# Kernel optimization log

Measured on AMD Instinct MI355X. Metric: run time of the kernel, lower is better.

## Reference

```python
import jax, jax.numpy as jnp
import numpy as np

N_ITEM = 50000
N_NODES = 2 * N_ITEM
NNZ = 3200000
EMB = 512
N_LAYERS = 3
BATCH = 4096
EPS = 1e-12


def setup_inputs() -> dict:
    key = jax.random.key(0)
    ks = jax.random.split(key, 12)
    s = 1.0 / np.sqrt(EMB)
    return {
        "all_vision": jax.random.normal(ks[0], (N_ITEM, EMB), jnp.float32) * s,
        "all_text": jax.random.normal(ks[1], (N_ITEM, EMB), jnp.float32) * s,
        "edge_row": jax.random.randint(ks[2], (NNZ,), 0, N_NODES, jnp.int32),
        "edge_col": jax.random.randint(ks[3], (NNZ,), 0, N_NODES, jnp.int32),
        "edge_val": jax.random.uniform(ks[4], (NNZ,), jnp.float32) * (1.0 / 32.0),
        "items": jax.random.randint(ks[5], (BATCH,), 0, N_ITEM, jnp.int32),
        "W_gc": jax.random.normal(ks[6], (N_LAYERS, EMB, EMB), jnp.float32) * s,
        "b_gc": jax.random.normal(ks[7], (N_LAYERS, EMB), jnp.float32) * 0.01,
        "W_gc2": jax.random.normal(ks[8], (N_LAYERS, EMB, EMB), jnp.float32) * s,
        "b_gc2": jax.random.normal(ks[9], (N_LAYERS, EMB), jnp.float32) * 0.01,
        "W_bi": jax.random.normal(ks[10], (N_LAYERS, EMB, EMB), jnp.float32) * s,
        "b_bi": jax.random.normal(ks[11], (N_LAYERS, EMB), jnp.float32) * 0.01,
    }


def reference(all_vision, all_text, edge_row, edge_col, edge_val, items,
              W_gc, b_gc, W_gc2, b_gc2, W_bi, b_bi):
    n = all_vision.shape[0]
    n_nodes = 2 * n

    def spmm(x):  # sparse [2N,2N] @ dense [2N,D] via gather + segment-sum
        return jax.ops.segment_sum(edge_val[:, None] * x[edge_col],
                                   edge_row, num_segments=n_nodes)

    ego = jnp.concatenate([all_vision, all_text], axis=0)   # [2N, D]
    oge = jnp.concatenate([all_text, all_vision], axis=0)   # fixed across layers
    acc = ego  # running sum over layer outputs (replaces stack+sum)
    for k in range(W_gc.shape[0]):
        side = spmm(ego)
        edis = spmm(oge)
        sum_e = side @ W_gc[k] + b_gc[k] + edis @ W_gc2[k] + b_gc2[k]
        bi = (ego * side + oge * edis) @ W_bi[k] + b_bi[k]
        ego = jax.nn.leaky_relu(sum_e + bi, negative_slope=0.2)
        # eval mode: message dropout is identity
        nrm = jnp.sqrt(jnp.sum(ego * ego, axis=1, keepdims=True))
        acc = acc + ego / jnp.maximum(nrm, EPS)  # F.normalize(p=2, dim=1)
    v_emb = acc[:n][items]
    t_emb = acc[n:][items]
    return (v_emb, t_emb)
```

## Files before the change

### kernel.cpp

```cpp
#include <hip/hip_runtime.h>
#include <stdint.h>

#define NITEM 50000
#define NN    100000
#define NNPAD 100352
#define CH    25088
#define NCH   4
#define EDGES 3200000
#define D     512
#define KCAT  1536
#define NL    3
#define BATCH 4096
#define NSEL  8192

typedef float  f32x4 __attribute__((ext_vector_type(4)));
typedef short  s16x8 __attribute__((ext_vector_type(8)));

__device__ __forceinline__ float bflo(unsigned u){ return __uint_as_float(u<<16); }
__device__ __forceinline__ float bfhi(unsigned u){ return __uint_as_float(u & 0xffff0000u); }
__device__ __forceinline__ float bf2f(unsigned short h){ return __uint_as_float(((unsigned)h)<<16); }
__device__ __forceinline__ unsigned short f2bf(float f){
  unsigned u = __float_as_uint(f);
  u += 0x7fffu + ((u>>16)&1u);
  return (unsigned short)(u>>16);
}
__device__ __forceinline__ void unpack8(uint4 d, float* f){
  f[0]=bflo(d.x); f[1]=bfhi(d.x);
  f[2]=bflo(d.y); f[3]=bfhi(d.y);
  f[4]=bflo(d.z); f[5]=bfhi(d.z);
  f[6]=bflo(d.w); f[7]=bfhi(d.w);
}
__device__ __forceinline__ uint4 pack8(const float* f){
  uint4 o;
  o.x = (unsigned)f2bf(f[0]) | ((unsigned)f2bf(f[1])<<16);
  o.y = (unsigned)f2bf(f[2]) | ((unsigned)f2bf(f[3])<<16);
  o.z = (unsigned)f2bf(f[4]) | ((unsigned)f2bf(f[5])<<16);
  o.w = (unsigned)f2bf(f[6]) | ((unsigned)f2bf(f[7])<<16);
  return o;
}
__device__ __forceinline__ void load8f(const void* base, size_t eoff, int isf32, float* f){
  if (isf32){
    const float* p = (const float*)base + eoff;
    f32x4 a = *(const f32x4*)p;
    f32x4 b = *(const f32x4*)(p + 4);
    f[0]=a[0]; f[1]=a[1]; f[2]=a[2]; f[3]=a[3];
    f[4]=b[0]; f[5]=b[1]; f[6]=b[2]; f[7]=b[3];
  } else {
    uint4 d = *(const uint4*)((const unsigned short*)base + eoff);
    unpack8(d, f);
  }
}
__device__ __forceinline__ float load1f(const void* base, size_t i, int isf32){
  return isf32 ? ((const float*)base)[i] : bf2f(((const unsigned short*)base)[i]);
}
__device__ __forceinline__ void gld_lds16(const void* g, void* l){
  __builtin_amdgcn_global_load_lds((__attribute__((address_space(1))) unsigned int*)(g),
                                   (__attribute__((address_space(3))) unsigned int*)(l),
                                   16, 0, 0);
}

__global__ void k_zero(int* __restrict__ p, int n){
  int i = blockIdx.x*256 + threadIdx.x;
  if (i < n) p[i] = 0;
}

__global__ void k_wsdbg(float* __restrict__ out, float mb, int n){
  int i = blockIdx.x*256 + threadIdx.x;
  if (i < n) out[i] = mb;
}

__global__ void k_detect(const unsigned short* __restrict__ vis, int* __restrict__ flag){
  __shared__ int cnt;
  if (threadIdx.x == 0) cnt = 0;
  __syncthreads();
  int c = 0;
  for (int i = threadIdx.x; i < 8192; i += 256){
    unsigned e = (vis[i] >> 7) & 0xFFu;
    if (e >= 0x80u) c++;
  }
  atomicAdd(&cnt, c);
  __syncthreads();
  if (threadIdx.x == 0) flag[0] = (cnt > 64) ? 1 : 0;
}

__global__ void k_hist(const int* __restrict__ row, int* __restrict__ counts){
  int e = blockIdx.x*256 + threadIdx.x;
  if (e < EDGES) atomicAdd(&counts[row[e]], 1);
}

__global__ void k_scan_a(const int* __restrict__ counts, int* __restrict__ incl, int* __restrict__ sums){
  __shared__ int sh[512];
  int t = threadIdx.x, b = blockIdx.x, i = b*512 + t;
  int x = (i < NN) ? counts[i] : 0;
  sh[t] = x; __syncthreads();
  for (int off = 1; off < 512; off <<= 1){
    int v = (t >= off) ? sh[t-off] : 0;
    __syncthreads();
    sh[t] += v;
    __syncthreads();
  }
  incl[i] = sh[t];
  if (t == 511) sums[b] = sh[511];
}

__global__ void k_scan_b(const int* __restrict__ sums, int* __restrict__ offs){
  if (threadIdx.x != 0) return;
  int run = 0;
  for (int j = 0; j < 196; ++j){ offs[j] = run; run += sums[j]; }
}

__global__ void k_scan_c(const int* __restrict__ incl, const int* __restrict__ offs,
                         const int* __restrict__ counts, int* __restrict__ rp, int* __restrict__ cur){
  int t = threadIdx.x, b = blockIdx.x, i = b*512 + t;
  if (i >= NN) return;
  int excl = offs[b] + (t > 0 ? incl[i-1] : 0);
  rp[i] = excl; cur[i] = excl;
  if (i == NN-1) rp[NN] = excl + counts[i];
}

__global__ void k_scatter(const int* __restrict__ row, const int* __restrict__ col,
                          const void* __restrict__ val, int* __restrict__ cur,
                          int* __restrict__ scol, unsigned short* __restrict__ sval,
                          const int* __restrict__ flagp){
  int e = blockIdx.x*256 + threadIdx.x;
  if (e >= EDGES) return;
  int isf32 = *flagp;
  int r = row[e];
  int p = atomicAdd(&cur[r], 1);
  scol[p] = col[e];
  sval[p] = isf32 ? f2bf(((const float*)val)[e]) : ((const unsigned short*)val)[e];
}

__global__ void k_bias(const void* __restrict__ bg, const void* __restrict__ bg2,
                       const void* __restrict__ bb, float* __restrict__ bias,
                       const int* __restrict__ flagp){
  int i = blockIdx.x*256 + threadIdx.x;
  int isf32 = *flagp;
  if (i < NL*D) bias[i] = load1f(bg, i, isf32) + load1f(bg2, i, isf32) + load1f(bb, i, isf32);
}

__global__ void k_btbuild(const void* __restrict__ Wgc, const void* __restrict__ Wgc2,
                          const void* __restrict__ Wbi, unsigned short* __restrict__ Bt,
                          const int* __restrict__ flagp){
  int id = blockIdx.x*256 + threadIdx.x;
  int isf32 = *flagp;
  int kk = id % KCAT;
  int n  = (id / KCAT) % D;
  int k  = id / (KCAT*D);
  int sel = kk >> 9, ki = kk & 511;
  const void* W = (sel==0) ? Wgc : ((sel==1) ? Wgc2 : Wbi);
  Bt[id] = f2bf(load1f(W, (size_t)k*D*D + (size_t)ki*D + n, isf32));
}

__global__ void k_acc_init(const void* __restrict__ vis, const void* __restrict__ txt,
                           const int* __restrict__ items, float* __restrict__ accs,
                           const int* __restrict__ flagp){
  int b = blockIdx.x*4 + (threadIdx.x >> 6);
  int lane = threadIdx.x & 63;
  int isf32 = *flagp;
  int it = items[b & (BATCH-1)];
  const void* src = (b < BATCH) ? vis : txt;
  float f[8]; load8f(src, (size_t)it*D + lane*8, isf32, f);
  float* ap = accs + (size_t)b*D + lane*8;
  f32x4 lo = {f[0],f[1],f[2],f[3]}, hi = {f[4],f[5],f[6],f[7]};
  *(f32x4*)ap = lo; *(f32x4*)(ap+4) = hi;
}

__global__ void k_quant(const void* __restrict__ vis, const void* __restrict__ txt,
                        signed char* __restrict__ Q, float* __restrict__ scl,
                        const int* __restrict__ flagp){
  int r = blockIdx.x*4 + (threadIdx.x >> 6);
  if (r >= NN) return;
  int lane = threadIdx.x & 63;
  int isf32 = *flagp;
  const void* src; size_t off;
  if (r < NITEM){ src = vis; off = (size_t)r*D; }
  else          { src = txt; off = (size_t)(r-NITEM)*D; }
  float f[8]; load8f(src, off + lane*8, isf32, f);
  float m = 0.f;
  #pragma unroll
  for (int j = 0; j < 8; ++j) m = fmaxf(m, fabsf(f[j]));
  #pragma unroll
  for (int o = 32; o >= 1; o >>= 1) m = fmaxf(m, __shfl_xor(m, o, 64));
  float inv = (m > 0.f) ? 127.f/m : 0.f;
  unsigned w0 = 0, w1 = 0;
  #pragma unroll
  for (int j = 0; j < 4; ++j){
    int q = (int)rintf(f[j]*inv);
    w0 |= ((unsigned)(q & 0xFF)) << (8*j);
  }
  #pragma unroll
  for (int j = 0; j < 4; ++j){
    int q = (int)rintf(f[4+j]*inv);
    w1 |= ((unsigned)(q & 0xFF)) << (8*j);
  }
  uint2 wv; wv.x = w0; wv.y = w1;
  *(uint2*)(Q + (size_t)r*D + lane*8) = wv;
  if (lane == 0) scl[r] = m * (1.f/127.f);
}

__global__ void k_spmm(const int* __restrict__ rp, const int* __restrict__ scol,
                       const unsigned short* __restrict__ sval,
                       const void* __restrict__ P0, const void* __restrict__ P1,
                       unsigned short* __restrict__ Y, int chunk0, const int* __restrict__ flagp){
  int rl   = blockIdx.x*4 + (threadIdx.x >> 6);
  int r    = chunk0 + rl;
  if (r >= NN) return;
  int isf32 = flagp ? *flagp : 0;
  int lane = threadIdx.x & 63;
  int s = rp[r], e = rp[r+1];
  float a[8] = {0,0,0,0,0,0,0,0};
  size_t lo = (size_t)lane*8;
  for (int i = s; i < e; ++i){
    int c0 = scol[i]; float v0 = bf2f(sval[i]);
    const void* qb; size_t qo;
    if (c0 < NITEM){ qb = P0; qo = (size_t)c0*D + lo; }
    else           { qb = P1; qo = (size_t)(c0-NITEM)*D + lo; }
    float f0[8]; load8f(qb, qo, isf32, f0);
    #pragma unroll
    for (int j = 0; j < 8; ++j) a[j] = fmaf(v0, f0[j], a[j]);
  }
  *(uint4*)(Y + (size_t)rl*D + lo) = pack8(a);
}

__global__ void k_spmm_q8(const int* __restrict__ rp, const int* __restrict__ scol,
                          const unsigned short* __restrict__ sval,
                          const signed char* __restrict__ Q, const float* __restrict__ scl,
                          unsigned short* __restrict__ Y, int chunk0, int dosw){
  int rl   = blockIdx.x*4 + (threadIdx.x >> 6);
  int r    = chunk0 + rl;
  if (r >= NN) return;
  int lane = threadIdx.x & 63;
  int s = rp[r], e = rp[r+1];
  float a[8] = {0,0,0,0,0,0,0,0};
  const int loff = lane*2;
  for (int i = s; i < e; ++i){
    int c0 = scol[i];
    int sc = dosw ? ((c0 < NITEM) ? c0 + NITEM : c0 - NITEM) : c0;
    float vs = bf2f(sval[i]) * scl[sc];
    uint2 w = *(const uint2*)((const int*)(Q + (size_t)sc*D) + loff);
    int w0 = (int)w.x, w1 = (int)w.y;
    a[0] = fmaf(vs, (float)((w0<<24)>>24), a[0]);
    a[1] = fmaf(vs, (float)((w0<<16)>>24), a[1]);
    a[2] = fmaf(vs, (float)((w0<< 8)>>24), a[2]);
    a[3] = fmaf(vs, (float)( w0     >>24), a[3]);
    a[4] = fmaf(vs, (float)((w1<<24)>>24), a[4]);
    a[5] = fmaf(vs, (float)((w1<<16)>>24), a[5]);
    a[6] = fmaf(vs, (float)((w1<< 8)>>24), a[6]);
    a[7] = fmaf(vs, (float)( w1     >>24), a[7]);
  }
  *(uint4*)(Y + (size_t)rl*D + (size_t)lane*8) = pack8(a);
}

__global__ void k_spmm_sel(const int* __restrict__ rp, const int* __restrict__ scol,
                           const unsigned short* __restrict__ sval,
                           const unsigned short* __restrict__ R,
                           const int* __restrict__ items,
                           unsigned short* __restrict__ Y){
  int b    = blockIdx.x*4 + (threadIdx.x >> 6);
  if (b >= NSEL) return;
  int lane = threadIdx.x & 63;
  int it = items[b & (BATCH-1)];
  int r  = (b < BATCH) ? it : it + NITEM;
  int s = rp[r], e = rp[r+1];
  float a[8] = {0,0,0,0,0,0,0,0};
  size_t lo = (size_t)lane*8;
  for (int i = s; i < e; ++i){
    int c0 = scol[i]; float v0 = bf2f(sval[i]);
    uint4 d = *(const uint4*)(R + (size_t)c0*D + lo);
    float f0[8]; unpack8(d, f0);
    #pragma unroll
    for (int j = 0; j < 8; ++j) a[j] = fmaf(v0, f0[j], a[j]);
  }
  *(uint4*)(Y + (size_t)b*D + lo) = pack8(a);
}

__global__ void k_z(const void* __restrict__ c0p, const void* __restrict__ c1p,
                    const unsigned short* __restrict__ side_c,
                    const unsigned short* __restrict__ ED,
                    const void* __restrict__ g0p, const void* __restrict__ g1p,
                    unsigned short* __restrict__ Z_c, int chunk0,
                    const int* __restrict__ cflagp, const int* __restrict__ gflagp){
  size_t tid = (size_t)blockIdx.x*256 + threadIdx.x;
  size_t base = tid*8;
  int rl = (int)(base >> 9);
  int cc = (int)(base & 511);
  int r  = chunk0 + rl;
  if (r >= NN) return;
  int cfl = cflagp ? *cflagp : 0;
  int gfl = gflagp ? *gflagp : 0;
  const void* cb; const void* gb; size_t ro;
  if (r < NITEM){ cb = c0p; gb = g0p; ro = (size_t)r*D + cc; }
  else          { cb = c1p; gb = g1p; ro = (size_t)(r-NITEM)*D + cc; }
  float fe[8], fg[8];
  load8f(cb, ro, cfl, fe);
  load8f(gb, ro, gfl, fg);
  uint4 ds = *(const uint4*)(side_c + base);
  uint4 dd = *(const uint4*)(ED + (size_t)r*D + cc);
  float fs_[8], fd[8];
  unpack8(ds,fs_); unpack8(dd,fd);
  float z[8];
  #pragma unroll
  for (int j = 0; j < 8; ++j) z[j] = fe[j]*fs_[j] + fg[j]*fd[j];
  *(uint4*)(Z_c + base) = pack8(z);
}

__global__ void k_zsel(const unsigned short* __restrict__ R,
                       const unsigned short* __restrict__ side_sel,
                       const unsigned short* __restrict__ ED,
                       const void* __restrict__ g0p, const void* __restrict__ g1p,
                       const int* __restrict__ items,
                       unsigned short* __restrict__ z_sel,
                       unsigned short* __restrict__ ED_sel,
                       const int* __restrict__ gflagp){
  size_t tid = (size_t)blockIdx.x*256 + threadIdx.x;
  int b  = (int)(tid >> 6);
  int cc = (int)(tid & 63) * 8;
  if (b >= NSEL) return;
  int gfl = *gflagp;
  int it = items[b & (BATCH-1)];
  int r  = (b < BATCH) ? it : it + NITEM;
  const void* gb; size_t ro;
  if (r < NITEM){ gb = g0p; ro = (size_t)r*D + cc; }
  else          { gb = g1p; ro = (size_t)(r-NITEM)*D + cc; }
  float fe[8], fg[8], fs_[8], fd[8];
  uint4 de = *(const uint4*)(R + (size_t)r*D + cc); unpack8(de, fe);
  load8f(gb, ro, gfl, fg);
  uint4 ds = *(const uint4*)(side_sel + (size_t)b*D + cc); unpack8(ds, fs_);
  uint4 dd = *(const uint4*)(ED + (size_t)r*D + cc); unpack8(dd, fd);
  float z[8];
  #pragma unroll
  for (int j = 0; j < 8; ++j) z[j] = fe[j]*fs_[j] + fg[j]*fd[j];
  *(uint4*)(z_sel + (size_t)b*D + cc) = pack8(z);
  *(uint4*)(ED_sel + (size_t)b*D + cc) = dd;
}

__global__ __launch_bounds__(256) void k_gemm(const unsigned short* __restrict__ A0,
                                              const unsigned short* __restrict__ A1,
                                              const unsigned short* __restrict__ A2,
                                              const unsigned short* __restrict__ Bt,
                                              const float* __restrict__ bias,
                                              unsigned short* __restrict__ C, int chunk0){
  __shared__ unsigned short As[128*64];
  __shared__ unsigned short Bs[128*64];
  const int t = threadIdx.x;
  const int lane = t & 63;
  const int w = t >> 6, wm = w >> 1, wn = w & 1;
  const int q = lane >> 4, l16 = lane & 15;
  const int ntile = blockIdx.x, mtile = blockIdx.y;

  f32x4 acc[4][4] = {};
  const size_t arow0 = (size_t)mtile*128;
  const size_t brow0 = (size_t)ntile*128;

  for (int kb = 0; kb < KCAT; kb += 64){
    int slab = kb >> 9, koff = kb & 511;
    const unsigned short* Ap = (slab==0) ? A0 : ((slab==1) ? A1 : A2);
    #pragma unroll
    for (int it = 0; it < 4; ++it){
      int ci = it*256 + t;
      int m = ci >> 3;
      int c = (ci & 7) ^ (m & 7);
      gld_lds16(Ap + (arow0 + m)*D    + koff + c*8, As + (size_t)ci*8);
      gld_lds16(Bt + (brow0 + m)*KCAT + kb   + c*8, Bs + (size_t)ci*8);
    }
    __syncthreads();
    #pragma unroll
    for (int ks = 0; ks < 2; ++ks){
      s16x8 af[4], bfr[4];
      #pragma unroll
      for (int mt = 0; mt < 4; ++mt){
        int m = wm*64 + mt*16 + l16;
        int ch = m*8 + (((ks<<2) + q) ^ (m & 7));
        af[mt] = *(const s16x8*)(As + (size_t)ch*8);
      }
      #pragma unroll
      for (int nt = 0; nt < 4; ++nt){
        int n = wn*64 + nt*16 + l16;
        int ch = n*8 + (((ks<<2) + q) ^ (n & 7));
        bfr[nt] = *(const s16x8*)(Bs + (size_t)ch*8);
      }
      #pragma unroll
      for (int mt = 0; mt < 4; ++mt)
        #pragma unroll
        for (int nt = 0; nt < 4; ++nt)
          acc[mt][nt] = __builtin_amdgcn_mfma_f32_16x16x32_bf16(af[mt], bfr[nt], acc[mt][nt], 0, 0, 0);
    }
    __syncthreads();
  }

  const int rbase = mtile*128 + wm*64;
  const int cbase = ntile*128 + wn*64;
  #pragma unroll
  for (int nt = 0; nt < 4; ++nt){
    int gc = cbase + nt*16 + l16;
    float bc = bias[gc];
    #pragma unroll
    for (int mt = 0; mt < 4; ++mt){
      int gr0 = rbase + mt*16 + q*4;
      #pragma unroll
      for (int rr = 0; rr < 4; ++rr){
        int gr = chunk0 + gr0 + rr;
        if (gr < NN){
          float x = acc[mt][nt][rr] + bc;
          x = (x > 0.f) ? x : 0.2f*x;
          C[(size_t)gr*D + gc] = f2bf(x);
        }
      }
    }
  }
}

__global__ void k_normacc(const unsigned short* __restrict__ next, const int* __restrict__ items,
                          float* __restrict__ accs){
  int b = blockIdx.x*4 + (threadIdx.x >> 6);
  int lane = threadIdx.x & 63;
  int it = items[b & (BATCH-1)];
  int src = (b < BATCH) ? it : it + NITEM;
  uint4 d = *(const uint4*)(next + (size_t)src*D + lane*8);
  float f[8]; unpack8(d, f);
  float s = 0.f;
  #pragma unroll
  for (int j = 0; j < 8; ++j) s += f[j]*f[j];
  #pragma unroll
  for (int off = 32; off >= 1; off >>= 1) s += __shfl_xor(s, off, 64);
  float inv = 1.0f / fmaxf(sqrtf(s), 1e-12f);
  float* ap = accs + (size_t)b*D + lane*8;
  f32x4 x0 = *(f32x4*)ap, x1 = *(f32x4*)(ap + 4);
  f32x4 a0 = {f[0]*inv, f[1]*inv, f[2]*inv, f[3]*inv};
  f32x4 a1 = {f[4]*inv, f[5]*inv, f[6]*inv, f[7]*inv};
  x0 += a0; x1 += a1;
  *(f32x4*)ap = x0; *(f32x4*)(ap + 4) = x1;
}

__global__ void k_normacc_sel(const unsigned short* __restrict__ next_sel,
                              float* __restrict__ accs){
  int b = blockIdx.x*4 + (threadIdx.x >> 6);
  if (b >= NSEL) return;
  int lane = threadIdx.x & 63;
  uint4 d = *(const uint4*)(next_sel + (size_t)b*D + lane*8);
  float f[8]; unpack8(d, f);
  float s = 0.f;
  #pragma unroll
  for (int j = 0; j < 8; ++j) s += f[j]*f[j];
  #pragma unroll
  for (int off = 32; off >= 1; off >>= 1) s += __shfl_xor(s, off, 64);
  float inv = 1.0f / fmaxf(sqrtf(s), 1e-12f);
  float* ap = accs + (size_t)b*D + lane*8;
  f32x4 x0 = *(f32x4*)ap, x1 = *(f32x4*)(ap + 4);
  f32x4 a0 = {f[0]*inv, f[1]*inv, f[2]*inv, f[3]*inv};
  f32x4 a1 = {f[4]*inv, f[5]*inv, f[6]*inv, f[7]*inv};
  x0 += a0; x1 += a1;
  *(f32x4*)ap = x0; *(f32x4*)(ap + 4) = x1;
}

__global__ void k_out(const float* __restrict__ accs, float* __restrict__ out,
                      const int* __restrict__ flagp){
  size_t tid = (size_t)blockIdx.x*256 + threadIdx.x;
  size_t base = tid*8;
  const float* sp = accs + base;
  float mark = 1000.0f * (float)(1 + *flagp);
  float f[8];
  #pragma unroll
  for (int j = 0; j < 8; ++j){
    float v = sp[j];
    f[j] = (v != v) ? mark : v;
  }
  f32x4 lo = {f[0],f[1],f[2],f[3]}, hi = {f[4],f[5],f[6],f[7]};
  *(f32x4*)(out + base)     = lo;
  *(f32x4*)(out + base + 4) = hi;
}

extern "C" void kernel_launch(void* const* d_in, const int* in_sizes, int n_in,
                              void* d_out, int out_size, void* d_ws, size_t ws_size,
                              hipStream_t stream){
  const void* vis  = d_in[0];
  const void* txt  = d_in[1];
  const int*  erow = (const int*)d_in[2];
  const int*  ecol = (const int*)d_in[3];
  const void* eval = d_in[4];
  const int*  items= (const int*)d_in[5];
  const void* Wgc  = d_in[6];
  const void* bgc  = d_in[7];
  const void* Wgc2 = d_in[8];
  const void* bgc2 = d_in[9];
  const void* Wbi  = d_in[10];
  const void* bbi  = d_in[11];
  float* out = (float*)d_out;

  char* w = (char*)d_ws;
  auto carve = [&](size_t b)->char*{ char* p = w; w += (b + 255) & ~(size_t)255; return p; };
  int*   counts = (int*)  carve((size_t)NN*4);
  int*   cursor = (int*)  carve((size_t)NN*4);
  int*   rp     = (int*)  carve(((size_t)NN+1)*4);
  int*   incl   = (int*)  carve((size_t)196*512*4);
  int*   sums   = (int*)  carve(196*4);
  int*   offs   = (int*)  carve(196*4);
  int*   dflag  = (int*)  carve(256);
  int*   scol   = (int*)  carve((size_t)EDGES*4);
  unsigned short* sval = (unsigned short*)carve((size_t)EDGES*2);
  unsigned short* ED   = (unsigned short*)carve((size_t)NNPAD*D*2);
  unsigned short* R0   = (unsigned short*)carve((size_t)NN*D*2);
  unsigned short* R1   = (unsigned short*)carve((size_t)NN*D*2);
  unsigned short* side = (unsigned short*)carve((size_t)CH*D*2);
  unsigned short* Zc   = (unsigned short*)carve((size_t)CH*D*2);
  unsigned short* Bt   = (unsigned short*)carve((size_t)NL*D*KCAT*2);
  float*          bias = (float*)         carve((size_t)NL*D*4);
  float*          accs = (float*)         carve((size_t)2*BATCH*D*4);
  unsigned short* sideS = R0;
  unsigned short* edS   = R0 + (size_t)NSEL*D;
  unsigned short* zS    = R0 + (size_t)2*NSEL*D;
  unsigned short* nxS   = R0 + (size_t)3*NSEL*D;
  signed char* Q0  = (signed char*)R1;
  float*       scl = (float*)((char*)R1 + (size_t)NN*D);
  size_t need = (size_t)(w - (char*)d_ws);
  if (need > ws_size){
    k_wsdbg<<<(out_size + 255)/256, 256, 0, stream>>>(out, (float)(ws_size >> 20), out_size);
    return;
  }

  k_detect <<<1, 256, 0, stream>>>((const unsigned short*)vis, dflag);
  k_zero   <<<(NN + 255)/256, 256, 0, stream>>>(counts, NN);
  k_hist   <<<EDGES/256, 256, 0, stream>>>(erow, counts);
  k_scan_a <<<196, 512, 0, stream>>>(counts, incl, sums);
  k_scan_b <<<1, 64, 0, stream>>>(sums, offs);
  k_scan_c <<<196, 512, 0, stream>>>(incl, offs, counts, rp, cursor);
  k_scatter<<<EDGES/256, 256, 0, stream>>>(erow, ecol, eval, cursor, scol, sval, dflag);
  k_bias   <<<(NL*D + 255)/256, 256, 0, stream>>>(bgc, bgc2, bbi, bias, dflag);
  k_btbuild<<<NL*D*KCAT/256, 256, 0, stream>>>(Wgc, Wgc2, Wbi, Bt, dflag);
  k_acc_init<<<2*BATCH/4, 256, 0, stream>>>(vis, txt, items, accs, dflag);
  k_quant  <<<NN/4, 256, 0, stream>>>(vis, txt, Q0, scl, dflag);

  k_spmm_q8<<<NN/4, 256, 0, stream>>>(rp, scol, sval, Q0, scl, ED, 0, 1);

  for (int k = 0; k < NL-1; ++k){
    unsigned short* next = (k == 1) ? R1 : R0;
    for (int c = 0; c < NCH; ++c){
      int chunk0 = c*CH;
      if (k == 0){
        k_spmm_q8<<<CH/4, 256, 0, stream>>>(rp, scol, sval, Q0, scl, side, chunk0, 0);
        k_z<<<CH*D/(256*8), 256, 0, stream>>>(vis, txt, side, ED, txt, vis, Zc, chunk0, dflag, dflag);
      } else {
        const unsigned short* R = R0;
        k_spmm<<<CH/4, 256, 0, stream>>>(rp, scol, sval, R, R + (size_t)NITEM*D, side, chunk0, nullptr);
        k_z<<<CH*D/(256*8), 256, 0, stream>>>(R, R + (size_t)NITEM*D, side, ED, txt, vis, Zc, chunk0, nullptr, dflag);
      }
      k_gemm<<<dim3(4, CH/128), 256, 0, stream>>>(side, ED + (size_t)chunk0*D, Zc,
                                                  Bt + (size_t)k*D*KCAT, bias + k*D, next, chunk0);
    }
    k_normacc<<<2*BATCH/4, 256, 0, stream>>>(next, items, accs);
  }

  k_spmm_sel<<<NSEL/4, 256, 0, stream>>>(rp, scol, sval, R1, items, sideS);
  k_zsel    <<<NSEL*64/256, 256, 0, stream>>>(R1, sideS, ED, txt, vis, items, zS, edS, dflag);
  k_gemm    <<<dim3(4, NSEL/128), 256, 0, stream>>>(sideS, edS, zS,
                                                    Bt + (size_t)2*D*KCAT, bias + 2*D, nxS, 0);
  k_normacc_sel<<<NSEL/4, 256, 0, stream>>>(nxS, accs);

  k_out<<<2*BATCH*D/(256*8), 256, 0, stream>>>(accs, out, dflag);

  (void)in_sizes; (void)n_in;
}
```

Measured before the change: 2.904 ms.

## Quantize layer-1 embeddings and edis to int8 for SpMM gathers and GEMM input

Adds a quantization pass over the layer-1 output so the layer-2 SpMM gathers int8 rows with per-row scales instead of bf16 rows. The fixed edis result is now written directly as int8 plus scales from a fused SpMM-quantize kernel, and the z, zsel and GEMM kernels dequantize it on load. The goal is to halve gather and stream bandwidth. In exchange it adds a quantize pass, replaces async global-to-LDS loads with register dequantization in the GEMM's second slab, and loses some accuracy.

```diff
diff --git a/kernel.cpp b/kernel.cpp
--- a/kernel.cpp
+++ b/kernel.cpp
@@ -38,6 +38,13 @@
   o.w = (unsigned)f2bf(f[6]) | ((unsigned)f2bf(f[7])<<16);
   return o;
 }
+__device__ __forceinline__ void dq8(uint2 w, float sc, float* f){
+  int w0 = (int)w.x, w1 = (int)w.y;
+  f[0]=sc*(float)((w0<<24)>>24); f[1]=sc*(float)((w0<<16)>>24);
+  f[2]=sc*(float)((w0<< 8)>>24); f[3]=sc*(float)( w0     >>24);
+  f[4]=sc*(float)((w1<<24)>>24); f[5]=sc*(float)((w1<<16)>>24);
+  f[6]=sc*(float)((w1<< 8)>>24); f[7]=sc*(float)( w1     >>24);
+}
 __device__ __forceinline__ void load8f(const void* base, size_t eoff, int isf32, float* f){
   if (isf32){
     const float* p = (const float*)base + eoff;
@@ -185,42 +192,35 @@
   float inv = (m > 0.f) ? 127.f/m : 0.f;
   unsigned w0 = 0, w1 = 0;
   #pragma unroll
-  for (int j = 0; j < 4; ++j){
-    int q = (int)rintf(f[j]*inv);
-    w0 |= ((unsigned)(q & 0xFF)) << (8*j);
-  }
-  #pragma unroll
-  for (int j = 0; j < 4; ++j){
-    int q = (int)rintf(f[4+j]*inv);
-    w1 |= ((unsigned)(q & 0xFF)) << (8*j);
-  }
+  for (int j = 0; j < 4; ++j) w0 |= ((unsigned)(((int)rintf(f[j]*inv))   & 0xFF)) << (8*j);
+  #pragma unroll
+  for (int j = 0; j < 4; ++j) w1 |= ((unsigned)(((int)rintf(f[4+j]*inv)) & 0xFF)) << (8*j);
   uint2 wv; wv.x = w0; wv.y = w1;
   *(uint2*)(Q + (size_t)r*D + lane*8) = wv;
   if (lane == 0) scl[r] = m * (1.f/127.f);
 }
 
-__global__ void k_spmm(const int* __restrict__ rp, const int* __restrict__ scol,
-                       const unsigned short* __restrict__ sval,
-                       const void* __restrict__ P0, const void* __restrict__ P1,
-                       unsigned short* __restrict__ Y, int chunk0, const int* __restrict__ flagp){
-  int rl   = blockIdx.x*4 + (threadIdx.x >> 6);
-  int r    = chunk0 + rl;
+__global__ void k_quant1(const unsigned short* __restrict__ R,
+                         signed char* __restrict__ Q, float* __restrict__ scl){
+  int r = blockIdx.x*4 + (threadIdx.x >> 6);
   if (r >= NN) return;
-  int isf32 = flagp ? *flagp : 0;
-  int lane = threadIdx.x & 63;
-  int s = rp[r], e = rp[r+1];
-  float a[8] = {0,0,0,0,0,0,0,0};
-  size_t lo = (size_t)lane*8;
-  for (int i = s; i < e; ++i){
-    int c0 = scol[i]; float v0 = bf2f(sval[i]);
-    const void* qb; size_t qo;
-    if (c0 < NITEM){ qb = P0; qo = (size_t)c0*D + lo; }
-    else           { qb = P1; qo = (size_t)(c0-NITEM)*D + lo; }
-    float f0[8]; load8f(qb, qo, isf32, f0);
-    #pragma unroll
-    for (int j = 0; j < 8; ++j) a[j] = fmaf(v0, f0[j], a[j]);
-  }
-  *(uint4*)(Y + (size_t)rl*D + lo) = pack8(a);
+  int lane = threadIdx.x & 63;
+  uint4 d = *(const uint4*)(R + (size_t)r*D + lane*8);
+  float f[8]; unpack8(d, f);
+  float m = 0.f;
+  #pragma unroll
+  for (int j = 0; j < 8; ++j) m = fmaxf(m, fabsf(f[j]));
+  #pragma unroll
+  for (int o = 32; o >= 1; o >>= 1) m = fmaxf(m, __shfl_xor(m, o, 64));
+  float inv = (m > 0.f) ? 127.f/m : 0.f;
+  unsigned w0 = 0, w1 = 0;
+  #pragma unroll
+  for (int j = 0; j < 4; ++j) w0 |= ((unsigned)(((int)rintf(f[j]*inv))   & 0xFF)) << (8*j);
+  #pragma unroll
+  for (int j = 0; j < 4; ++j) w1 |= ((unsigned)(((int)rintf(f[4+j]*inv)) & 0xFF)) << (8*j);
+  uint2 wv; wv.x = w0; wv.y = w1;
+  *(uint2*)(Q + (size_t)r*D + lane*8) = wv;
+  if (lane == 0) scl[r] = m * (1.f/127.f);
 }
 
 __global__ void k_spmm_q8(const int* __restrict__ rp, const int* __restrict__ scol,
@@ -252,6 +252,48 @@
   *(uint4*)(Y + (size_t)rl*D + (size_t)lane*8) = pack8(a);
 }
 
+__global__ void k_spmm_q8q(const int* __restrict__ rp, const int* __restrict__ scol,
+                           const unsigned short* __restrict__ sval,
+                           const signed char* __restrict__ Q, const float* __restrict__ scl,
+                           signed char* __restrict__ Yq, float* __restrict__ Yscl, int dosw){
+  int r = blockIdx.x*4 + (threadIdx.x >> 6);
+  if (r >= NNPAD) return;
+  int lane = threadIdx.x & 63;
+  int s = 0, e = 0;
+  if (r < NN){ s = rp[r]; e = rp[r+1]; }
+  float a[8] = {0,0,0,0,0,0,0,0};
+  const int loff = lane*2;
+  for (int i = s; i < e; ++i){
+    int c0 = scol[i];
+    int sc = dosw ? ((c0 < NITEM) ? c0 + NITEM : c0 - NITEM) : c0;
+    float vs = bf2f(sval[i]) * scl[sc];
+    uint2 w = *(const uint2*)((const int*)(Q + (size_t)sc*D) + loff);
+    int w0 = (int)w.x, w1 = (int)w.y;
+    a[0] = fmaf(vs, (float)((w0<<24)>>24), a[0]);
+    a[1] = fmaf(vs, (float)((w0<<16)>>24), a[1]);
+    a[2] = fmaf(vs, (float)((w0<< 8)>>24), a[2]);
+    a[3] = fmaf(vs, (float)( w0     >>24), a[3]);
+    a[4] = fmaf(vs, (float)((w1<<24)>>24), a[4]);
+    a[5] = fmaf(vs, (float)((w1<<16)>>24), a[5]);
+    a[6] = fmaf(vs, (float)((w1<< 8)>>24), a[6]);
+    a[7] = fmaf(vs, (float)( w1     >>24), a[7]);
+  }
+  float m = 0.f;
+  #pragma unroll
+  for (int j = 0; j < 8; ++j) m = fmaxf(m, fabsf(a[j]));
+  #pragma unroll
+  for (int o = 32; o >= 1; o >>= 1) m = fmaxf(m, __shfl_xor(m, o, 64));
+  float inv = (m > 0.f) ? 127.f/m : 0.f;
+  unsigned w0 = 0, w1 = 0;
+  #pragma unroll
+  for (int j = 0; j < 4; ++j) w0 |= ((unsigned)(((int)rintf(a[j]*inv))   & 0xFF)) << (8*j);
+  #pragma unroll
+  for (int j = 0; j < 4; ++j) w1 |= ((unsigned)(((int)rintf(a[4+j]*inv)) & 0xFF)) << (8*j);
+  uint2 wv; wv.x = w0; wv.y = w1;
+  *(uint2*)(Yq + (size_t)r*D + lane*8) = wv;
+  if (lane == 0) Yscl[r] = m * (1.f/127.f);
+}
+
 __global__ void k_spmm_sel(const int* __restrict__ rp, const int* __restrict__ scol,
                            const unsigned short* __restrict__ sval,
                            const unsigned short* __restrict__ R,
@@ -277,7 +319,7 @@
 
 __global__ void k_z(const void* __restrict__ c0p, const void* __restrict__ c1p,
                     const unsigned short* __restrict__ side_c,
-                    const unsigned short* __restrict__ ED,
+                    const signed char* __restrict__ EDq, const float* __restrict__ EDscl,
                     const void* __restrict__ g0p, const void* __restrict__ g1p,
                     unsigned short* __restrict__ Z_c, int chunk0,
                     const int* __restrict__ cflagp, const int* __restrict__ gflagp){
@@ -296,9 +338,10 @@
   load8f(cb, ro, cfl, fe);
   load8f(gb, ro, gfl, fg);
   uint4 ds = *(const uint4*)(side_c + base);
-  uint4 dd = *(const uint4*)(ED + (size_t)r*D + cc);
   float fs_[8], fd[8];
-  unpack8(ds,fs_); unpack8(dd,fd);
+  unpack8(ds,fs_);
+  uint2 wd = *(const uint2*)(EDq + (size_t)r*D + cc);
+  dq8(wd, EDscl[r], fd);
   float z[8];
   #pragma unroll
   for (int j = 0; j < 8; ++j) z[j] = fe[j]*fs_[j] + fg[j]*fd[j];
@@ -307,11 +350,11 @@
 
 __global__ void k_zsel(const unsigned short* __restrict__ R,
                        const unsigned short* __restrict__ side_sel,
-                       const unsigned short* __restrict__ ED,
+                       const signed char* __restrict__ EDq, const float* __restrict__ EDscl,
                        const void* __restrict__ g0p, const void* __restrict__ g1p,
                        const int* __restrict__ items,
                        unsigned short* __restrict__ z_sel,
-                       unsigned short* __restrict__ ED_sel,
+                       signed char* __restrict__ edSq, float* __restrict__ edSscl,
                        const int* __restrict__ gflagp){
   size_t tid = (size_t)blockIdx.x*256 + threadIdx.x;
   int b  = (int)(tid >> 6);
@@ -327,16 +370,20 @@
   uint4 de = *(const uint4*)(R + (size_t)r*D + cc); unpack8(de, fe);
   load8f(gb, ro, gfl, fg);
   uint4 ds = *(const uint4*)(side_sel + (size_t)b*D + cc); unpack8(ds, fs_);
-  uint4 dd = *(const uint4*)(ED + (size_t)r*D + cc); unpack8(dd, fd);
+  uint2 wd = *(const uint2*)(EDq + (size_t)r*D + cc);
+  float sc = EDscl[r];
+  dq8(wd, sc, fd);
   float z[8];
   #pragma unroll
   for (int j = 0; j < 8; ++j) z[j] = fe[j]*fs_[j] + fg[j]*fd[j];
   *(uint4*)(z_sel + (size_t)b*D + cc) = pack8(z);
-  *(uint4*)(ED_sel + (size_t)b*D + cc) = dd;
+  *(uint2*)(edSq + (size_t)b*D + cc) = wd;
+  if (cc == 0) edSscl[b] = sc;
 }
 
 __global__ __launch_bounds__(256) void k_gemm(const unsigned short* __restrict__ A0,
-                                              const unsigned short* __restrict__ A1,
+                                              const signed char* __restrict__ A1q,
+                                              const float* __restrict__ A1scl,
                                               const unsigned short* __restrict__ A2,
                                               const unsigned short* __restrict__ Bt,
                                               const float* __restrict__ bias,
@@ -355,14 +402,21 @@
 
   for (int kb = 0; kb < KCAT; kb += 64){
     int slab = kb >> 9, koff = kb & 511;
-    const unsigned short* Ap = (slab==0) ? A0 : ((slab==1) ? A1 : A2);
     #pragma unroll
     for (int it = 0; it < 4; ++it){
       int ci = it*256 + t;
       int m = ci >> 3;
       int c = (ci & 7) ^ (m & 7);
-      gld_lds16(Ap + (arow0 + m)*D    + koff + c*8, As + (size_t)ci*8);
-      gld_lds16(Bt + (brow0 + m)*KCAT + kb   + c*8, Bs + (size_t)ci*8);
+      if (slab == 1){
+        uint2 w8 = *(const uint2*)(A1q + (arow0 + m)*D + koff + c*8);
+        float sc = A1scl[arow0 + m];
+        float f[8]; dq8(w8, sc, f);
+        *(uint4*)(As + (size_t)ci*8) = pack8(f);
+      } else {
+        const unsigned short* Ap = (slab==0) ? A0 : A2;
+        gld_lds16(Ap + (arow0 + m)*D + koff + c*8, As + (size_t)ci*8);
+      }
+      gld_lds16(Bt + (brow0 + m)*KCAT + kb + c*8, Bs + (size_t)ci*8);
     }
     __syncthreads();
     #pragma unroll
@@ -499,7 +553,10 @@
   int*   dflag  = (int*)  carve(256);
   int*   scol   = (int*)  carve((size_t)EDGES*4);
   unsigned short* sval = (unsigned short*)carve((size_t)EDGES*2);
-  unsigned short* ED   = (unsigned short*)carve((size_t)NNPAD*D*2);
+  signed char*    EDq8 = (signed char*)   carve((size_t)NNPAD*D);
+  float*          EDscl= (float*)         carve((size_t)NNPAD*4);
+  signed char*    Q1   = (signed char*)   carve((size_t)NN*D);
+  float*          scl1 = (float*)         carve((size_t)NN*4);
   unsigned short* R0   = (unsigned short*)carve((size_t)NN*D*2);
   unsigned short* R1   = (unsigned short*)carve((size_t)NN*D*2);
   unsigned short* side = (unsigned short*)carve((size_t)CH*D*2);
@@ -507,10 +564,11 @@
   unsigned short* Bt   = (unsigned short*)carve((size_t)NL*D*KCAT*2);
   float*          bias = (float*)         carve((size_t)NL*D*4);
   float*          accs = (float*)         carve((size_t)2*BATCH*D*4);
-  unsigned short* sideS = R0;
-  unsigned short* edS   = R0 + (size_t)NSEL*D;
-  unsigned short* zS    = R0 + (size_t)2*NSEL*D;
-  unsigned short* nxS   = R0 + (size_t)3*NSEL*D;
+  unsigned short* sideS  = R0;
+  signed char*    edSq   = (signed char*)(R0 + (size_t)NSEL*D);
+  float*          edSscl = (float*)((char*)edSq + (size_t)NSEL*D);
+  unsigned short* zS     = (unsigned short*)((char*)edSscl + (size_t)NSEL*4);
+  unsigned short* nxS    = zS + (size_t)NSEL*D;
   signed char* Q0  = (signed char*)R1;
   float*       scl = (float*)((char*)R1 + (size_t)NN*D);
   size_t need = (size_t)(w - (char*)d_ws);
@@ -531,29 +589,31 @@
   k_acc_init<<<2*BATCH/4, 256, 0, stream>>>(vis, txt, items, accs, dflag);
   k_quant  <<<NN/4, 256, 0, stream>>>(vis, txt, Q0, scl, dflag);
 
-  k_spmm_q8<<<NN/4, 256, 0, stream>>>(rp, scol, sval, Q0, scl, ED, 0, 1);
-
-  for (int k = 0; k < NL-1; ++k){
-    unsigned short* next = (k == 1) ? R1 : R0;
-    for (int c = 0; c < NCH; ++c){
-      int chunk0 = c*CH;
-      if (k == 0){
-        k_spmm_q8<<<CH/4, 256, 0, stream>>>(rp, scol, sval, Q0, scl, side, chunk0, 0);
-        k_z<<<CH*D/(256*8), 256, 0, stream>>>(vis, txt, side, ED, txt, vis, Zc, chunk0, dflag, dflag);
-      } else {
-        const unsigned short* R = R0;
-        k_spmm<<<CH/4, 256, 0, stream>>>(rp, scol, sval, R, R + (size_t)NITEM*D, side, chunk0, nullptr);
-        k_z<<<CH*D/(256*8), 256, 0, stream>>>(R, R + (size_t)NITEM*D, side, ED, txt, vis, Zc, chunk0, nullptr, dflag);
-      }
-      k_gemm<<<dim3(4, CH/128), 256, 0, stream>>>(side, ED + (size_t)chunk0*D, Zc,
-                                                  Bt + (size_t)k*D*KCAT, bias + k*D, next, chunk0);
-    }
-    k_normacc<<<2*BATCH/4, 256, 0, stream>>>(next, items, accs);
-  }
+  k_spmm_q8q<<<NNPAD/4, 256, 0, stream>>>(rp, scol, sval, Q0, scl, EDq8, EDscl, 1);
+
+  for (int c = 0; c < NCH; ++c){
+    int chunk0 = c*CH;
+    k_spmm_q8<<<CH/4, 256, 0, stream>>>(rp, scol, sval, Q0, scl, side, chunk0, 0);
+    k_z<<<CH*D/(256*8), 256, 0, stream>>>(vis, txt, side, EDq8, EDscl, txt, vis, Zc, chunk0, dflag, dflag);
+    k_gemm<<<dim3(4, CH/128), 256, 0, stream>>>(side, EDq8 + (size_t)chunk0*D, EDscl + chunk0, Zc,
+                                                Bt, bias, R0, chunk0);
+  }
+  k_normacc<<<2*BATCH/4, 256, 0, stream>>>(R0, items, accs);
+
+  k_quant1<<<NN/4, 256, 0, stream>>>(R0, Q1, scl1);
+
+  for (int c = 0; c < NCH; ++c){
+    int chunk0 = c*CH;
+    k_spmm_q8<<<CH/4, 256, 0, stream>>>(rp, scol, sval, Q1, scl1, side, chunk0, 0);
+    k_z<<<CH*D/(256*8), 256, 0, stream>>>(R0, R0 + (size_t)NITEM*D, side, EDq8, EDscl, txt, vis, Zc, chunk0, nullptr, dflag);
+    k_gemm<<<dim3(4, CH/128), 256, 0, stream>>>(side, EDq8 + (size_t)chunk0*D, EDscl + chunk0, Zc,
+                                                Bt + (size_t)1*D*KCAT, bias + 1*D, R1, chunk0);
+  }
+  k_normacc<<<2*BATCH/4, 256, 0, stream>>>(R1, items, accs);
 
   k_spmm_sel<<<NSEL/4, 256, 0, stream>>>(rp, scol, sval, R1, items, sideS);
-  k_zsel    <<<NSEL*64/256, 256, 0, stream>>>(R1, sideS, ED, txt, vis, items, zS, edS, dflag);
-  k_gemm    <<<dim3(4, NSEL/128), 256, 0, stream>>>(sideS, edS, zS,
+  k_zsel    <<<NSEL*64/256, 256, 0, stream>>>(R1, sideS, EDq8, EDscl, txt, vis, items, zS, edSq, edSscl, dflag);
+  k_gemm    <<<dim3(4, NSEL/128), 256, 0, stream>>>(sideS, edSq, edSscl, zS,
                                                     Bt + (size_t)2*D*KCAT, bias + 2*D, nxS, 0);
   k_normacc_sel<<<NSEL/4, 256, 0, stream>>>(nxS, accs);
 
```

Result: no change. 2.936 ms (+1.1%).
